# Kernel optimization log

Measured on AMD Instinct MI355X. Metric: run time of the kernel, lower is better.

## Reference

```python
import jax, jax.numpy as jnp
import numpy as np

N_NODES = 5000
N_EDGES = 40000
NUM_ATOM_TYPES = 100
HID = 32            # multiplicity of 0e and 1o in irreps_hidden
EDGE_ATTR_DIM = 8
NUM_BOND_TYPES = 5
OUT_SCALARS = 2 * 6 + 1  # max_charge=6 -> 13x0e
CUTOFF = 5.0
SQRT3 = 1.7320508075688772


def _sh(edge_vec):
    # o3.SphericalHarmonics('1x0e + 1x1o', normalize=True, normalization='component')
    d = jnp.sqrt(jnp.sum(edge_vec * edge_vec, axis=-1) + 1e-12)
    n = edge_vec / d[:, None]
    sh0 = jnp.ones(edge_vec.shape[0], edge_vec.dtype)          # [E]
    sh1 = SQRT3 * n[:, (1, 2, 0)]                              # [E,3], e3nn (y,z,x) order
    return sh0, sh1, d


def _soft_one_hot(d):
    # e3nn.math.soft_one_hot_linspace(d, 0, cutoff, 8, basis='gaussian', cutoff=True)
    values = jnp.linspace(0.0, CUTOFF, EDGE_ATTR_DIM + 2)[1:-1]
    step = CUTOFF / (EDGE_ATTR_DIM + 1)
    diff = (d[:, None] - values[None, :]) / step
    return jnp.exp(-diff * diff) / 1.12


def _mlp(x, W0, b0, W1, b1):
    # ScalarMLP(in, out, hidden=[in], SiLU)
    return jax.nn.silu(x @ W0 + b0) @ W1 + b1


def _tp_init(s, sh0, sh1, w):
    # FCTP(32x0e, 1x0e+1x1o -> 32x0e+32x1o); paths: 0e*0e->0e, 0e*1o->1o
    E = s.shape[0]
    w1 = w[:, : HID * HID].reshape(E, HID, HID)
    w2 = w[:, HID * HID :].reshape(E, HID, HID)
    c = 1.0 / np.sqrt(HID)  # fan-in = 32 per output irrep
    out_s = c * jnp.einsum('eu,euw->ew', s * sh0[:, None], w1)
    out_v = c * jnp.einsum('eu,ei,euw->ewi', s, sh1, w2)
    return out_s, out_v


def _tp_hidden(s, v, sh0, sh1, w):
    # FCTP(32x0e+32x1o, 1x0e+1x1o -> 32x0e+32x1o)
    # path order: 0e*0e->0e, 0e*1o->1o, 1o*0e->1o, 1o*1o->0e
    E = s.shape[0]
    ws = w.reshape(E, 4, HID, HID)
    c = 1.0 / np.sqrt(2 * HID)  # fan-in = 64 per output irrep
    dot = jnp.einsum('eui,ei->eu', v, sh1) / SQRT3  # CG(1,1->0) = delta/sqrt(3)
    out_s = c * (jnp.einsum('eu,euw->ew', s * sh0[:, None], ws[:, 0]) +
                 jnp.einsum('eu,euw->ew', dot, ws[:, 3]))
    out_v = c * (jnp.einsum('eu,ei,euw->ewi', s, sh1, ws[:, 1]) +
                 jnp.einsum('eui,euw->ewi', v * sh0[:, None, None], ws[:, 2]))
    return out_s, out_v


def _edge_tp(s1, v1, s2, v2, sh0, sh1, w):
    # FCTP(64x0e+64x1o (concat of two hidden), 1x0e+1x1o -> 5x0e)
    # blocks in concat order: s_src, v_src, s_dst, v_dst
    E = s1.shape[0]
    ws = w.reshape(E, 4, HID, NUM_BOND_TYPES)
    c = 1.0 / np.sqrt(4 * HID)  # fan-in = 128
    d1 = jnp.einsum('eui,ei->eu', v1, sh1) / SQRT3
    d2 = jnp.einsum('eui,ei->eu', v2, sh1) / SQRT3
    return c * (jnp.einsum('eu,euw->ew', s1 * sh0[:, None], ws[:, 0]) +
                jnp.einsum('eu,euw->ew', d1, ws[:, 1]) +
                jnp.einsum('eu,euw->ew', s2 * sh0[:, None], ws[:, 2]) +
                jnp.einsum('eu,euw->ew', d2, ws[:, 3]))


def _scatter_mean(ms, mv, dst, n):
    cnt = jax.ops.segment_sum(jnp.ones(dst.shape[0], ms.dtype), dst, num_segments=n)
    cnt = jnp.maximum(cnt, 1.0)
    s = jax.ops.segment_sum(ms, dst, num_segments=n) / cnt[:, None]
    v = jax.ops.segment_sum(mv, dst, num_segments=n) / cnt[:, None, None]
    return s, v


def setup_inputs() -> dict:
    key = jax.random.key(0)
    ks = jax.random.split(key, 16)
    def w(k, shape, fan_in):
        return jax.random.normal(k, shape, dtype=jnp.float32) / np.sqrt(fan_in)
    inp = {}
    inp['coordinates'] = jax.random.normal(ks[0], (N_NODES, 3), dtype=jnp.float32) * 1.5
    inp['atom_types'] = jax.random.randint(ks[1], (N_NODES,), 0, NUM_ATOM_TYPES)
    inp['edge_index'] = jax.random.randint(ks[2], (2, N_EDGES), 0, N_NODES)
    inp['atom_embed'] = jax.random.normal(ks[3], (NUM_ATOM_TYPES, HID), dtype=jnp.float32)
    inp['ip_W0'] = w(ks[4], (EDGE_ATTR_DIM, EDGE_ATTR_DIM), EDGE_ATTR_DIM)
    inp['ip_b0'] = jnp.zeros((EDGE_ATTR_DIM,), jnp.float32)
    inp['ip_W1'] = w(ks[5], (EDGE_ATTR_DIM, 2 * HID * HID), EDGE_ATTR_DIM)
    inp['ip_b1'] = jnp.zeros((2 * HID * HID,), jnp.float32)
    inp['ly_W0'] = w(ks[6], (EDGE_ATTR_DIM, EDGE_ATTR_DIM), EDGE_ATTR_DIM)
    inp['ly_b0'] = jnp.zeros((EDGE_ATTR_DIM,), jnp.float32)
    inp['ly_W1'] = w(ks[7], (EDGE_ATTR_DIM, 4 * HID * HID), EDGE_ATTR_DIM)
    inp['ly_b1'] = jnp.zeros((4 * HID * HID,), jnp.float32)
    inp['ly_Ws'] = jax.random.normal(ks[8], (HID, HID), dtype=jnp.float32)
    inp['ly_Wv'] = jax.random.normal(ks[9], (HID, HID), dtype=jnp.float32)
    inp['et_W0'] = w(ks[10], (EDGE_ATTR_DIM, EDGE_ATTR_DIM), EDGE_ATTR_DIM)
    inp['et_b0'] = jnp.zeros((EDGE_ATTR_DIM,), jnp.float32)
    inp['et_W1'] = w(ks[11], (EDGE_ATTR_DIM, 4 * HID * NUM_BOND_TYPES), EDGE_ATTR_DIM)
    inp['et_b1'] = jnp.zeros((4 * HID * NUM_BOND_TYPES,), jnp.float32)
    inp['no_W1'] = jax.random.normal(ks[12], (HID, OUT_SCALARS), dtype=jnp.float32)
    inp['no_W2'] = jax.random.normal(ks[13], (OUT_SCALARS, OUT_SCALARS), dtype=jnp.float32)
    return inp


def reference(coordinates, atom_types, edge_index, atom_embed,
              ip_W0, ip_b0, ip_W1, ip_b1,
              ly_W0, ly_b0, ly_W1, ly_b1, ly_Ws, ly_Wv,
              et_W0, et_b0, et_W1, et_b1, no_W1, no_W2):
    n = coordinates.shape[0]
    src, dst = edge_index[0], edge_index[1]
    edge_vec = coordinates[dst] - coordinates[src]
    sh0, sh1, d = _sh(edge_vec)
    edge_attr = _soft_one_hot(d)                              # [E,8]
    # initial projector: Conv(32x0e -> 32x0e+32x1o)
    s0 = atom_embed[atom_types]                               # [N,32]
    w_ip = _mlp(edge_attr, ip_W0, ip_b0, ip_W1, ip_b1)        # [E,2048]
    ms, mv = _tp_init(s0[src], sh0, sh1, w_ip)
    s, v = _scatter_mean(ms, mv, dst, n)                      # [N,32],[N,32,3]
    # one LinearSelfInteraction(Conv) layer
    w_ly = _mlp(edge_attr, ly_W0, ly_b0, ly_W1, ly_b1)        # [E,4096]
    ms, mv = _tp_hidden(s[src], v[src], sh0, sh1, w_ly)
    cs, cv = _scatter_mean(ms, mv, dst, n)
    lc = 1.0 / np.sqrt(HID)  # e3nn o3.Linear normalization
    s = cs + lc * (s @ ly_Ws)
    v = cv + lc * jnp.einsum('eui,uw->ewi', v, ly_Wv)
    # edge output: FCTP([h_src, h_dst], edge_sh) with radial weights
    w_et = _mlp(edge_attr, et_W0, et_b0, et_W1, et_b1)        # [E,640]
    edge_out = _edge_tp(s[src], v[src], s[dst], v[dst], sh0, sh1, w_et)  # [E,5]
    # node output MLP on detached scalar channel (13x0e)
    sd = jax.lax.stop_gradient(s)
    h = jax.nn.silu(sd @ no_W1 / np.sqrt(HID))
    node_out = h @ no_W2 / np.sqrt(OUT_SCALARS)               # [N,13]
    return edge_out, node_out
```

## Files before the change

### kernel.cpp

```cpp
#include <hip/hip_runtime.h>

#define NN 5000
#define NE 40000

typedef unsigned int u32;
typedef unsigned short u16;
typedef __attribute__((ext_vector_type(8))) short bf16x8;
typedef __attribute__((ext_vector_type(4))) float f32x4;

union ABfrag { uint4 q; bf16x8 v; u32 u[4]; };

__device__ __forceinline__ float siluf(float x) { return x / (1.f + __expf(-x)); }

__device__ __forceinline__ u32 f2bf_u(float f) {
  u32 x = __float_as_uint(f);
  return (x + 0x7FFFu + ((x >> 16) & 1u)) >> 16;
}
__device__ __forceinline__ u16 f2bf(float f) { return (u16)f2bf_u(f); }
__device__ __forceinline__ float bf2f(u16 v) { return __uint_as_float(((u32)v) << 16); }
__device__ __forceinline__ u32 packbf2(float lo, float hi) {
  return f2bf_u(lo) | (f2bf_u(hi) << 16);
}
__device__ __forceinline__ u32 pk2(float a, float b) {
  return ((__float_as_uint(a) + 0x8000u) >> 16) |
         ((__float_as_uint(b) + 0x8000u) & 0xFFFF0000u);
}
__device__ __forceinline__ void pksplit8(const float* p, ABfrag& hi, ABfrag& lo) {
#pragma unroll
  for (int j = 0; j < 8; j += 2) {
    u32 h2 = pk2(p[j], p[j+1]);
    hi.u[j >> 1] = h2;
    float h0 = __uint_as_float(h2 << 16);
    float h1 = __uint_as_float(h2 & 0xFFFF0000u);
    lo.u[j >> 1] = pk2(p[j] - h0, p[j+1] - h1);
  }
}
__device__ __forceinline__ void unpack8(uint4 q, float* f) {
  f[0] = __uint_as_float(q.x << 16); f[1] = __uint_as_float(q.x & 0xFFFF0000u);
  f[2] = __uint_as_float(q.y << 16); f[3] = __uint_as_float(q.y & 0xFFFF0000u);
  f[4] = __uint_as_float(q.z << 16); f[5] = __uint_as_float(q.z & 0xFFFF0000u);
  f[6] = __uint_as_float(q.w << 16); f[7] = __uint_as_float(q.w & 0xFFFF0000u);
}
__device__ __forceinline__ float dot8f(const float* h, const float* w, float init) {
  float a = init;
#pragma unroll
  for (int k = 0; k < 8; k++) a = fmaf(h[k], w[k], a);
  return a;
}
__device__ __forceinline__ void mlp8(const float* ea, const float* __restrict__ W0,
                                     const float* __restrict__ b0, float* h) {
#pragma unroll
  for (int j = 0; j < 8; j++) {
    float a = b0[j];
#pragma unroll
    for (int i = 0; i < 8; i++) a += ea[i] * W0[i*8 + j];
    h[j] = siluf(a);
  }
}

__global__ void k_geom(const float* __restrict__ coords, const int* __restrict__ eidx,
                       const float* __restrict__ ipW0, const float* __restrict__ ipb0,
                       const float* __restrict__ lyW0, const float* __restrict__ lyb0,
                       const float* __restrict__ etW0, const float* __restrict__ etb0,
                       float* __restrict__ sh, float* __restrict__ h_ip,
                       float* __restrict__ h_ly, float* __restrict__ h_et,
                       int* __restrict__ cur, int* __restrict__ perm) {
  int e = blockIdx.x * blockDim.x + threadIdx.x;
  if (e >= NE) return;
  int s = eidx[e], d = eidx[NE + e];
  float vx = coords[d*3+0] - coords[s*3+0];
  float vy = coords[d*3+1] - coords[s*3+1];
  float vz = coords[d*3+2] - coords[s*3+2];
  float dist = sqrtf(vx*vx + vy*vy + vz*vz + 1e-12f);
  float inv = 1.f / dist;
  const float SQ3 = 1.7320508075688772f;
  sh[e*3+0] = SQ3 * vy * inv;
  sh[e*3+1] = SQ3 * vz * inv;
  sh[e*3+2] = SQ3 * vx * inv;
  float ea[8];
  const float step = 5.f / 9.f;
#pragma unroll
  for (int j = 0; j < 8; j++) {
    float diff = (dist - step * (float)(j+1)) * (9.f / 5.f);
    ea[j] = __expf(-diff*diff) * (1.f / 1.12f);
  }
  float h[8];
  mlp8(ea, ipW0, ipb0, h);
#pragma unroll
  for (int j = 0; j < 8; j++) h_ip[e*8+j] = h[j];
  mlp8(ea, lyW0, lyb0, h);
#pragma unroll
  for (int j = 0; j < 8; j++) h_ly[e*8+j] = h[j];
  mlp8(ea, etW0, etb0, h);
#pragma unroll
  for (int j = 0; j < 8; j++) h_et[e*8+j] = h[j];
  int t = atomicAdd(&cur[d], 1);
  if (t < 64) perm[d*64 + t] = e;
}

__global__ __launch_bounds__(256) void k_mconv1(
    const float* __restrict__ hE, const float* __restrict__ sh,
    const float* __restrict__ sIn, const int* __restrict__ atype,
    const int* __restrict__ eidx,
    const float* __restrict__ W1, const float* __restrict__ b1,
    int ldw, float cscale, u16* __restrict__ msg) {
  __shared__ u16 B[64*296];
  {
    int col = threadIdx.x & 63, p = col >> 5, w = col & 31;
    int k0 = (threadIdx.x >> 6) * 72;
    for (int k = k0; k < k0 + 72; k++) {
      float v = (k < 256) ? W1[(k >> 5)*ldw + p*1024 + (k & 31)*32 + w]
                          : b1[p*1024 + (k - 256)*32 + w];
      B[col*296 + k] = f2bf(v);
    }
  }
  __syncthreads();
  int tile = blockIdx.x*4 + (threadIdx.x >> 6);
  if (tile*16 >= NE) return;
  int lane = threadIdx.x & 63;
  int m = lane & 15, q = lane >> 4;
  int e = tile*16 + m;
  int srcn = eidx[e];
  int srow = atype ? atype[srcn] : srcn;
  float4 sA = *(const float4*)&sIn[srow*32 + q*8];
  float4 sB = *(const float4*)&sIn[srow*32 + q*8 + 4];
  float4 hA = *(const float4*)&hE[e*8];
  float4 hB = *(const float4*)&hE[e*8 + 4];
  float sf[8] = {sA.x,sA.y,sA.z,sA.w,sB.x,sB.y,sB.z,sB.w};
  float hf[8] = {hA.x,hA.y,hA.z,hA.w,hB.x,hB.y,hB.z,hB.w};
  f32x4 acc0 = {0.f,0.f,0.f,0.f}, acc1 = acc0, acc2 = acc0, acc3 = acc0;
#pragma unroll
  for (int ks = 0; ks < 9; ks++) {
    float hs = (ks < 8) ? hf[ks] : 1.f;
    float pr[8];
#pragma unroll
    for (int j = 0; j < 8; j++) pr[j] = hs * sf[j];
    ABfrag ahi, alo;
    pksplit8(pr, ahi, alo);
    int kb = ks*32 + q*8;
    ABfrag b0, b1f, b2, b3;
    b0.q  = *(const uint4*)&B[( 0 + m)*296 + kb];
    b1f.q = *(const uint4*)&B[(16 + m)*296 + kb];
    b2.q  = *(const uint4*)&B[(32 + m)*296 + kb];
    b3.q  = *(const uint4*)&B[(48 + m)*296 + kb];
    acc0 = __builtin_amdgcn_mfma_f32_16x16x32_bf16(ahi.v, b0.v,  acc0, 0, 0, 0);
    acc0 = __builtin_amdgcn_mfma_f32_16x16x32_bf16(alo.v, b0.v,  acc0, 0, 0, 0);
    acc1 = __builtin_amdgcn_mfma_f32_16x16x32_bf16(ahi.v, b1f.v, acc1, 0, 0, 0);
    acc1 = __builtin_amdgcn_mfma_f32_16x16x32_bf16(alo.v, b1f.v, acc1, 0, 0, 0);
    acc2 = __builtin_amdgcn_mfma_f32_16x16x32_bf16(ahi.v, b2.v,  acc2, 0, 0, 0);
    acc2 = __builtin_amdgcn_mfma_f32_16x16x32_bf16(alo.v, b2.v,  acc2, 0, 0, 0);
    acc3 = __builtin_amdgcn_mfma_f32_16x16x32_bf16(ahi.v, b3.v,  acc3, 0, 0, 0);
    acc3 = __builtin_amdgcn_mfma_f32_16x16x32_bf16(alo.v, b3.v,  acc3, 0, 0, 0);
  }
#pragma unroll
  for (int r = 0; r < 4; r++) {
    int et = tile*16 + q*4 + r;
    u16* mp = msg + (size_t)et*128;
    mp[m]      = f2bf(cscale*acc0[r]);
    mp[16 + m] = f2bf(cscale*acc1[r]);
    float s0v = sh[et*3+0], s1v = sh[et*3+1], s2v = sh[et*3+2];
    float m0 = cscale*acc2[r], m1 = cscale*acc3[r];
    mp[32 +      m] = f2bf(m0*s0v);
    mp[64 +      m] = f2bf(m0*s1v);
    mp[96 +      m] = f2bf(m0*s2v);
    mp[32 + 16 + m] = f2bf(m1*s0v);
    mp[64 + 16 + m] = f2bf(m1*s1v);
    mp[96 + 16 + m] = f2bf(m1*s2v);
  }
}

__global__ __launch_bounds__(256) void k_conv2(
    const float* __restrict__ hE, const float* __restrict__ sh,
    const float* __restrict__ s1, const float* __restrict__ v1soa,
    const int* __restrict__ eidx,
    const float* __restrict__ W1, const float* __restrict__ b1,
    u16* __restrict__ msgA, u16* __restrict__ msgB) {
  __shared__ u16 B[64*296];
  const bool scalarHalf = blockIdx.x < 625;
  int blk = scalarHalf ? blockIdx.x : blockIdx.x - 625;
  if (scalarHalf) {
    int col = threadIdx.x & 63, p = col >> 5, w = col & 31;
    int k0 = (threadIdx.x >> 6) * 72;
    for (int k = k0; k < k0 + 72; k++) {
      float v = (k < 256) ? W1[(k >> 5)*4096 + p*1024 + (k & 31)*32 + w]
                          : b1[p*1024 + (k - 256)*32 + w];
      B[col*296 + k] = f2bf(v);
    }
  } else {
    int col = threadIdx.x & 63;
    int base = (col < 32) ? (2048 + col) : (3072 + (col - 32));
    int k0 = (threadIdx.x >> 6) * 72;
    for (int k = k0; k < k0 + 72; k++) {
      float v = (k < 256) ? W1[(k >> 5)*4096 + base + (k & 31)*32]
                          : b1[base + (k - 256)*32];
      B[col*296 + k] = f2bf(v);
    }
  }
  __syncthreads();
  int tile = blk*4 + (threadIdx.x >> 6);
  if (tile*16 >= NE) return;
  int lane = threadIdx.x & 63;
  int m = lane & 15, q = lane >> 4;
  int e = tile*16 + m;
  int srcn = eidx[e];
  float4 hA = *(const float4*)&hE[e*8];
  float4 hB = *(const float4*)&hE[e*8 + 4];
  float hf[8] = {hA.x,hA.y,hA.z,hA.w,hB.x,hB.y,hB.z,hB.w};
  const float c = 0.125f;

  if (scalarHalf) {
    float4 sA = *(const float4*)&s1[srcn*32 + q*8];
    float4 sB = *(const float4*)&s1[srcn*32 + q*8 + 4];
    float sf[8] = {sA.x,sA.y,sA.z,sA.w,sB.x,sB.y,sB.z,sB.w};
    f32x4 acc0 = {0.f,0.f,0.f,0.f}, acc1 = acc0, acc2 = acc0, acc3 = acc0;
#pragma unroll
    for (int ks = 0; ks < 9; ks++) {
      float hs = (ks < 8) ? hf[ks] : 1.f;
      float pr[8];
#pragma unroll
      for (int j = 0; j < 8; j++) pr[j] = hs * sf[j];
      ABfrag ahi, alo;
      pksplit8(pr, ahi, alo);
      int kb = ks*32 + q*8;
      ABfrag b0, b1f, b2, b3;
      b0.q  = *(const uint4*)&B[( 0 + m)*296 + kb];
      b1f.q = *(const uint4*)&B[(16 + m)*296 + kb];
      b2.q  = *(const uint4*)&B[(32 + m)*296 + kb];
      b3.q  = *(const uint4*)&B[(48 + m)*296 + kb];
      acc0 = __builtin_amdgcn_mfma_f32_16x16x32_bf16(ahi.v, b0.v,  acc0, 0, 0, 0);
      acc0 = __builtin_amdgcn_mfma_f32_16x16x32_bf16(alo.v, b0.v,  acc0, 0, 0, 0);
      acc1 = __builtin_amdgcn_mfma_f32_16x16x32_bf16(ahi.v, b1f.v, acc1, 0, 0, 0);
      acc1 = __builtin_amdgcn_mfma_f32_16x16x32_bf16(alo.v, b1f.v, acc1, 0, 0, 0);
      acc2 = __builtin_amdgcn_mfma_f32_16x16x32_bf16(ahi.v, b2.v,  acc2, 0, 0, 0);
      acc2 = __builtin_amdgcn_mfma_f32_16x16x32_bf16(alo.v, b2.v,  acc2, 0, 0, 0);
      acc3 = __builtin_amdgcn_mfma_f32_16x16x32_bf16(ahi.v, b3.v,  acc3, 0, 0, 0);
      acc3 = __builtin_amdgcn_mfma_f32_16x16x32_bf16(alo.v, b3.v,  acc3, 0, 0, 0);
    }
#pragma unroll
    for (int r = 0; r < 4; r++) {
      int et = tile*16 + q*4 + r;
      u16* mp = msgA + (size_t)et*128;
      mp[m]      = f2bf(c*acc0[r]);
      mp[16 + m] = f2bf(c*acc1[r]);
      float s0v = sh[et*3+0], s1v = sh[et*3+1], s2v = sh[et*3+2];
      float m0 = c*acc2[r], m1 = c*acc3[r];
      mp[32 +      m] = f2bf(m0*s0v);
      mp[64 +      m] = f2bf(m0*s1v);
      mp[96 +      m] = f2bf(m0*s2v);
      mp[32 + 16 + m] = f2bf(m1*s0v);
      mp[64 + 16 + m] = f2bf(m1*s1v);
      mp[96 + 16 + m] = f2bf(m1*s2v);
    }
  } else {
    const float is3 = 0.5773502691896258f;
    float vf[3][8];
#pragma unroll
    for (int i = 0; i < 3; i++) {
      float4 aa = *(const float4*)&v1soa[i*160000 + srcn*32 + q*8];
      float4 bb = *(const float4*)&v1soa[i*160000 + srcn*32 + q*8 + 4];
      vf[i][0]=aa.x; vf[i][1]=aa.y; vf[i][2]=aa.z; vf[i][3]=aa.w;
      vf[i][4]=bb.x; vf[i][5]=bb.y; vf[i][6]=bb.z; vf[i][7]=bb.w;
    }
    float es0 = sh[e*3+0], es1 = sh[e*3+1], es2 = sh[e*3+2];
    float df[8];
#pragma unroll
    for (int j = 0; j < 8; j++)
      df[j] = (vf[0][j]*es0 + vf[1][j]*es1 + vf[2][j]*es2) * is3;
    f32x4 z = {0.f,0.f,0.f,0.f};
    f32x4 aV00 = z, aV01 = z, aV10 = z, aV11 = z, aV20 = z, aV21 = z, aD0 = z, aD1 = z;
#pragma unroll
    for (int ks = 0; ks < 9; ks++) {
      int kb = ks*32 + q*8;
      ABfrag b0, b1f, b2, b3;
      b0.q  = *(const uint4*)&B[( 0 + m)*296 + kb];
      b1f.q = *(const uint4*)&B[(16 + m)*296 + kb];
      b2.q  = *(const uint4*)&B[(32 + m)*296 + kb];
      b3.q  = *(const uint4*)&B[(48 + m)*296 + kb];
      float hs = (ks < 8) ? hf[ks] : 1.f;
      float pr[8];
      ABfrag hi, lo;
#pragma unroll
      for (int j = 0; j < 8; j++) pr[j] = hs * vf[0][j];
      pksplit8(pr, hi, lo);
      aV00 = __builtin_amdgcn_mfma_f32_16x16x32_bf16(hi.v, b0.v,  aV00, 0, 0, 0);
      aV00 = __builtin_amdgcn_mfma_f32_16x16x32_bf16(lo.v, b0.v,  aV00, 0, 0, 0);
      aV01 = __builtin_amdgcn_mfma_f32_16x16x32_bf16(hi.v, b1f.v, aV01, 0, 0, 0);
      aV01 = __builtin_amdgcn_mfma_f32_16x16x32_bf16(lo.v, b1f.v, aV01, 0, 0, 0);
#pragma unroll
      for (int j = 0; j < 8; j++) pr[j] = hs * vf[1][j];
      pksplit8(pr, hi, lo);
      aV10 = __builtin_amdgcn_mfma_f32_16x16x32_bf16(hi.v, b0.v,  aV10, 0, 0, 0);
      aV10 = __builtin_amdgcn_mfma_f32_16x16x32_bf16(lo.v, b0.v,  aV10, 0, 0, 0);
      aV11 = __builtin_amdgcn_mfma_f32_16x16x32_bf16(hi.v, b1f.v, aV11, 0, 0, 0);
      aV11 = __builtin_amdgcn_mfma_f32_16x16x32_bf16(lo.v, b1f.v, aV11, 0, 0, 0);
#pragma unroll
      for (int j = 0; j < 8; j++) pr[j] = hs * vf[2][j];
      pksplit8(pr, hi, lo);
      aV20 = __builtin_amdgcn_mfma_f32_16x16x32_bf16(hi.v, b0.v,  aV20, 0, 0, 0);
      aV20 = __builtin_amdgcn_mfma_f32_16x16x32_bf16(lo.v, b0.v,  aV20, 0, 0, 0);
      aV21 = __builtin_amdgcn_mfma_f32_16x16x32_bf16(hi.v, b1f.v, aV21, 0, 0, 0);
      aV21 = __builtin_amdgcn_mfma_f32_16x16x32_bf16(lo.v, b1f.v, aV21, 0, 0, 0);
#pragma unroll
      for (int j = 0; j < 8; j++) pr[j] = hs * df[j];
      pksplit8(pr, hi, lo);
      aD0  = __builtin_amdgcn_mfma_f32_16x16x32_bf16(hi.v, b2.v,  aD0,  0, 0, 0);
      aD0  = __builtin_amdgcn_mfma_f32_16x16x32_bf16(lo.v, b2.v,  aD0,  0, 0, 0);
      aD1  = __builtin_amdgcn_mfma_f32_16x16x32_bf16(hi.v, b3.v,  aD1,  0, 0, 0);
      aD1  = __builtin_amdgcn_mfma_f32_16x16x32_bf16(lo.v, b3.v,  aD1,  0, 0, 0);
    }
#pragma unroll
    for (int r = 0; r < 4; r++) {
      int et = tile*16 + q*4 + r;
      u16* mp = msgB + (size_t)et*128;
      mp[m]      = f2bf(c*aD0[r]);
      mp[16 + m] = f2bf(c*aD1[r]);
      mp[32 +      m] = f2bf(c*aV00[r]);
      mp[32 + 16 + m] = f2bf(c*aV01[r]);
      mp[64 +      m] = f2bf(c*aV10[r]);
      mp[64 + 16 + m] = f2bf(c*aV11[r]);
      mp[96 +      m] = f2bf(c*aV20[r]);
      mp[96 + 16 + m] = f2bf(c*aV21[r]);
    }
  }
}

__global__ void k_gather1(const u16* __restrict__ msg, const int* __restrict__ perm,
                          const int* __restrict__ cur, float* __restrict__ s1,
                          float* __restrict__ v1soa) {
  int t = blockIdx.x * blockDim.x + threadIdx.x;
  int n = t >> 7, c = t & 127;
  if (n >= NN) return;
  int deg = min(cur[n], 64);
  float acc = 0.f;
  for (int j = 0; j < deg; j++) {
    int e = perm[n*64 + j];
    acc += bf2f(msg[(size_t)e*128 + c]);
  }
  acc /= (float)max(deg, 1);
  if (c < 32) s1[n*32 + c] = acc;
  else { int i = (c-32) >> 5, w = (c-32) & 31; v1soa[i*160000 + n*32 + w] = acc; }
}

__global__ __launch_bounds__(256) void k_gather2(
    const u16* __restrict__ msgA, const u16* __restrict__ msgB,
    const int* __restrict__ perm, const int* __restrict__ cur,
    const float* __restrict__ s1, const float* __restrict__ v1soa,
    const float* __restrict__ Ws, const float* __restrict__ Wv,
    const float* __restrict__ noW1, const float* __restrict__ noW2,
    float* __restrict__ s2, float* __restrict__ v2, float* __restrict__ outN) {
  __shared__ float sb[2][32];
  __shared__ float hb[2][13];
  int t = blockIdx.x * blockDim.x + threadIdx.x;
  int n = t >> 7, c = t & 127;
  int ln = (threadIdx.x >> 7);
  int deg = min(cur[n], 64);
  float acc = 0.f;
  for (int j = 0; j < deg; j++) {
    int e = perm[n*64 + j];
    acc += bf2f(msgA[(size_t)e*128 + c]) + bf2f(msgB[(size_t)e*128 + c]);
  }
  acc /= (float)max(deg, 1);
  const float lc = 0.17677669529663687f;
  if (c < 32) {
    float ss = 0.f;
#pragma unroll 8
    for (int u = 0; u < 32; u++) ss += s1[n*32 + u] * Ws[u*32 + c];
    float val = acc + lc*ss;
    s2[n*32 + c] = val;
    sb[ln][c] = val;
  } else {
    int i = (c-32) >> 5, w = (c-32) & 31;
    float sv = 0.f;
#pragma unroll 8
    for (int u = 0; u < 32; u++) sv += v1soa[i*160000 + n*32 + u] * Wv[u*32 + w];
    v2[n*96 + w*3 + i] = acc + lc*sv;
  }
  __syncthreads();
  const float i32 = 0.17677669529663687f;
  if (c < 13) {
    float a = 0.f;
#pragma unroll 8
    for (int u = 0; u < 32; u++) a += sb[ln][u] * noW1[u*13 + c];
    hb[ln][c] = siluf(a * i32);
  }
  __syncthreads();
  const float i13 = 0.2773500981126146f;
  if (c < 13) {
    float a = 0.f;
#pragma unroll
    for (int j = 0; j < 13; j++) a += hb[ln][j] * noW2[j*13 + c];
    outN[n*13 + c] = a * i13;
  }
}

__global__ __launch_bounds__(256) void k_e3(
    const float* __restrict__ hE, const float* __restrict__ sh,
    const float* __restrict__ s2, const float* __restrict__ v2,
    const int* __restrict__ eidx,
    const float* __restrict__ W1, const float* __restrict__ b1,
    float* __restrict__ out) {
  __shared__ uint4 WQ[640];
  __shared__ float BQ[640];
  for (int t = threadIdx.x; t < 640; t += 256) {
    int u = t & 31, pw = t >> 5, p2 = pw / 5, w = pw - p2*5;
    int col = p2*160 + u*5 + w;
    const float* s = W1 + col;
    uint4 q;
    q.x = packbf2(s[0],      s[640]);
    q.y = packbf2(s[1280],   s[1920]);
    q.z = packbf2(s[2560],   s[3200]);
    q.w = packbf2(s[3840],   s[4480]);
    WQ[t] = q;
    BQ[t] = b1[col];
  }
  __syncthreads();
  const int g = threadIdx.x >> 5, tw = threadIdx.x & 31;
  const float c = 0.08838834764831845f;
  const float is3 = 0.5773502691896258f;
  for (int p = blockIdx.x*8 + g; p*2 < NE; p += gridDim.x*8) {
    int e0 = p*2, e1 = e0 + 1;
    float h0[8], h1[8];
    {
      float4 qa = *(const float4*)&hE[e0*8];
      float4 qb = *(const float4*)&hE[e0*8+4];
      h0[0]=qa.x; h0[1]=qa.y; h0[2]=qa.z; h0[3]=qa.w;
      h0[4]=qb.x; h0[5]=qb.y; h0[6]=qb.z; h0[7]=qb.w;
      float4 qc = *(const float4*)&hE[e1*8];
      float4 qd = *(const float4*)&hE[e1*8+4];
      h1[0]=qc.x; h1[1]=qc.y; h1[2]=qc.z; h1[3]=qc.w;
      h1[4]=qd.x; h1[5]=qd.y; h1[6]=qd.z; h1[7]=qd.w;
    }
    int sA = eidx[e0], dA = eidx[NE+e0];
    int sB = eidx[e1], dB = eidx[NE+e1];
    float sa0 = sh[e0*3+0], sa1 = sh[e0*3+1], sa2 = sh[e0*3+2];
    float sb0 = sh[e1*3+0], sb1 = sh[e1*3+1], sb2 = sh[e1*3+2];
    float c00 = s2[sA*32 + tw];
    float c01 = (v2[sA*96+tw*3+0]*sa0 + v2[sA*96+tw*3+1]*sa1 + v2[sA*96+tw*3+2]*sa2) * is3;
    float c02 = s2[dA*32 + tw];
    float c03 = (v2[dA*96+tw*3+0]*sa0 + v2[dA*96+tw*3+1]*sa1 + v2[dA*96+tw*3+2]*sa2) * is3;
    float c10 = s2[sB*32 + tw];
    float c11 = (v2[sB*96+tw*3+0]*sb0 + v2[sB*96+tw*3+1]*sb1 + v2[sB*96+tw*3+2]*sb2) * is3;
    float c12 = s2[dB*32 + tw];
    float c13 = (v2[dB*96+tw*3+0]*sb0 + v2[dB*96+tw*3+1]*sb1 + v2[dB*96+tw*3+2]*sb2) * is3;
    float part0[5] = {0,0,0,0,0};
    float part1[5] = {0,0,0,0,0};
#pragma unroll
    for (int pp = 0; pp < 4; pp++) {
      float cp0 = (pp==0) ? c00 : (pp==1) ? c01 : (pp==2) ? c02 : c03;
      float cp1 = (pp==0) ? c10 : (pp==1) ? c11 : (pp==2) ? c12 : c13;
#pragma unroll
      for (int w = 0; w < 5; w++) {
        int idx = (pp*5 + w)*32 + tw;
        float f[8];
        unpack8(WQ[idx], f);
        float bv = BQ[idx];
        part0[w] = fmaf(cp0, dot8f(h0, f, bv), part0[w]);
        part1[w] = fmaf(cp1, dot8f(h1, f, bv), part1[w]);
      }
    }
#pragma unroll
    for (int off = 16; off > 0; off >>= 1)
#pragma unroll
      for (int w = 0; w < 5; w++) {
        part0[w] += __shfl_xor(part0[w], off, 32);
        part1[w] += __shfl_xor(part1[w], off, 32);
      }
    float outv = 0.f;
#pragma unroll
    for (int w = 0; w < 5; w++) {
      if (tw == w)     outv = part0[w];
      if (tw == 5 + w) outv = part1[w];
    }
    if (tw < 10) out[e0*5 + tw] = c * outv;
  }
}

extern "C" void kernel_launch(void* const* d_in, const int* in_sizes, int n_in,
                              void* d_out, int out_size, void* d_ws, size_t ws_size,
                              hipStream_t stream) {
  (void)in_sizes; (void)n_in; (void)out_size; (void)ws_size;
  const float* coords = (const float*)d_in[0];
  const int*   atype  = (const int*)d_in[1];
  const int*   eidx   = (const int*)d_in[2];
  const float* emb    = (const float*)d_in[3];
  const float* ipW0 = (const float*)d_in[4];
  const float* ipb0 = (const float*)d_in[5];
  const float* ipW1 = (const float*)d_in[6];
  const float* ipb1 = (const float*)d_in[7];
  const float* lyW0 = (const float*)d_in[8];
  const float* lyb0 = (const float*)d_in[9];
  const float* lyW1 = (const float*)d_in[10];
  const float* lyb1 = (const float*)d_in[11];
  const float* lyWs = (const float*)d_in[12];
  const float* lyWv = (const float*)d_in[13];
  const float* etW0 = (const float*)d_in[14];
  const float* etb0 = (const float*)d_in[15];
  const float* etW1 = (const float*)d_in[16];
  const float* etb1 = (const float*)d_in[17];
  const float* noW1 = (const float*)d_in[18];
  const float* noW2 = (const float*)d_in[19];

  float* ws = (float*)d_ws;
  float* sh    = ws;
  float* h_ip  = ws + 120000;
  float* h_ly  = ws + 440000;
  float* h_et  = ws + 760000;
  float* s1    = ws + 1240000;
  float* v1soa = ws + 1400000;
  float* s2    = ws + 1880000;
  float* v2    = ws + 2040000;
  int*   cur   = (int*)(ws + 2520000);
  int*   perm  = (int*)(ws + 2525000);
  u16*   msgA  = (u16*)(ws + 2845000);
  u16*   msgB  = (u16*)(ws + 5405000);

  float* outE = (float*)d_out;
  float* outN = (float*)d_out + NE*5;

  hipMemsetAsync(cur, 0, (size_t)NN * sizeof(int), stream);
  k_geom<<<(NE + 255)/256, 256, 0, stream>>>(coords, eidx, ipW0, ipb0, lyW0, lyb0,
                                             etW0, etb0, sh, h_ip, h_ly, h_et, cur, perm);
  k_mconv1<<<625, 256, 0, stream>>>(h_ip, sh, emb, atype, eidx, ipW1, ipb1, 2048,
                                    0.17677669529663687f, msgA);
  k_gather1<<<(NN*128 + 255)/256, 256, 0, stream>>>(msgA, perm, cur, s1, v1soa);
  k_conv2<<<1250, 256, 0, stream>>>(h_ly, sh, s1, v1soa, eidx, lyW1, lyb1, msgA, msgB);
  k_gather2<<<2500, 256, 0, stream>>>(msgA, msgB, perm, cur, s1, v1soa,
                                      lyWs, lyWv, noW1, noW2, s2, v2, outN);
  k_e3<<<1024, 256, 0, stream>>>(h_et, sh, s2, v2, eidx, etW1, etb1, outE);
}
```

Baseline: 205.1 us.

## Switch conv MFMA to single-pass fp16 with persistent blocks and fragment-major LDS

```diff
diff --git a/kernel.cpp b/kernel.cpp
--- a/kernel.cpp
+++ b/kernel.cpp
@@ -5,10 +5,11 @@
 
 typedef unsigned int u32;
 typedef unsigned short u16;
-typedef __attribute__((ext_vector_type(8))) short bf16x8;
+typedef __fp16 h16x2 __attribute__((ext_vector_type(2)));
+typedef _Float16 f16x8 __attribute__((ext_vector_type(8)));
 typedef __attribute__((ext_vector_type(4))) float f32x4;
 
-union ABfrag { uint4 q; bf16x8 v; u32 u[4]; };
+union AF { u32 u[4]; f16x8 v; uint4 q; };
 
 __device__ __forceinline__ float siluf(float x) { return x / (1.f + __expf(-x)); }
 
@@ -21,19 +22,14 @@
 __device__ __forceinline__ u32 packbf2(float lo, float hi) {
   return f2bf_u(lo) | (f2bf_u(hi) << 16);
 }
-__device__ __forceinline__ u32 pk2(float a, float b) {
-  return ((__float_as_uint(a) + 0x8000u) >> 16) |
-         ((__float_as_uint(b) + 0x8000u) & 0xFFFF0000u);
-}
-__device__ __forceinline__ void pksplit8(const float* p, ABfrag& hi, ABfrag& lo) {
-#pragma unroll
-  for (int j = 0; j < 8; j += 2) {
-    u32 h2 = pk2(p[j], p[j+1]);
-    hi.u[j >> 1] = h2;
-    float h0 = __uint_as_float(h2 << 16);
-    float h1 = __uint_as_float(h2 & 0xFFFF0000u);
-    lo.u[j >> 1] = pk2(p[j] - h0, p[j+1] - h1);
-  }
+__device__ __forceinline__ u32 pkh2(float a, float b) {
+  union { h16x2 h; u32 u; } r;
+  r.h = __builtin_amdgcn_cvt_pkrtz(a, b);
+  return r.u;
+}
+__device__ __forceinline__ u16 f2h(float v) {
+  _Float16 h = (_Float16)v;
+  return *(u16*)&h;
 }
 __device__ __forceinline__ void unpack8(uint4 q, float* f) {
   f[0] = __uint_as_float(q.x << 16); f[1] = __uint_as_float(q.x & 0xFFFF0000u);
@@ -56,6 +52,14 @@
     for (int i = 0; i < 8; i++) a += ea[i] * W0[i*8 + j];
     h[j] = siluf(a);
   }
+}
+__device__ __forceinline__ AF mkfrag(float hs, const float* s) {
+  AF a;
+  a.u[0] = pkh2(hs*s[0], hs*s[1]);
+  a.u[1] = pkh2(hs*s[2], hs*s[3]);
+  a.u[2] = pkh2(hs*s[4], hs*s[5]);
+  a.u[3] = pkh2(hs*s[6], hs*s[7]);
+  return a;
 }
 
 __global__ void k_geom(const float* __restrict__ coords, const int* __restrict__ eidx,
@@ -104,222 +108,182 @@
     const int* __restrict__ eidx,
     const float* __restrict__ W1, const float* __restrict__ b1,
     int ldw, float cscale, u16* __restrict__ msg) {
-  __shared__ u16 B[64*296];
+  __shared__ __align__(16) u16 B2[36*64*8];
   {
     int col = threadIdx.x & 63, p = col >> 5, w = col & 31;
     int k0 = (threadIdx.x >> 6) * 72;
     for (int k = k0; k < k0 + 72; k++) {
       float v = (k < 256) ? W1[(k >> 5)*ldw + p*1024 + (k & 31)*32 + w]
                           : b1[p*1024 + (k - 256)*32 + w];
-      B[col*296 + k] = f2bf(v);
+      B2[((k >> 3)*64 + col)*8 + (k & 7)] = f2h(v);
     }
   }
   __syncthreads();
-  int tile = blockIdx.x*4 + (threadIdx.x >> 6);
-  if (tile*16 >= NE) return;
   int lane = threadIdx.x & 63;
-  int m = lane & 15, q = lane >> 4;
-  int e = tile*16 + m;
-  int srcn = eidx[e];
-  int srow = atype ? atype[srcn] : srcn;
-  float4 sA = *(const float4*)&sIn[srow*32 + q*8];
-  float4 sB = *(const float4*)&sIn[srow*32 + q*8 + 4];
-  float4 hA = *(const float4*)&hE[e*8];
-  float4 hB = *(const float4*)&hE[e*8 + 4];
-  float sf[8] = {sA.x,sA.y,sA.z,sA.w,sB.x,sB.y,sB.z,sB.w};
-  float hf[8] = {hA.x,hA.y,hA.z,hA.w,hB.x,hB.y,hB.z,hB.w};
-  f32x4 acc0 = {0.f,0.f,0.f,0.f}, acc1 = acc0, acc2 = acc0, acc3 = acc0;
-#pragma unroll
-  for (int ks = 0; ks < 9; ks++) {
-    float hs = (ks < 8) ? hf[ks] : 1.f;
-    float pr[8];
-#pragma unroll
-    for (int j = 0; j < 8; j++) pr[j] = hs * sf[j];
-    ABfrag ahi, alo;
-    pksplit8(pr, ahi, alo);
-    int kb = ks*32 + q*8;
-    ABfrag b0, b1f, b2, b3;
-    b0.q  = *(const uint4*)&B[( 0 + m)*296 + kb];
-    b1f.q = *(const uint4*)&B[(16 + m)*296 + kb];
-    b2.q  = *(const uint4*)&B[(32 + m)*296 + kb];
-    b3.q  = *(const uint4*)&B[(48 + m)*296 + kb];
-    acc0 = __builtin_amdgcn_mfma_f32_16x16x32_bf16(ahi.v, b0.v,  acc0, 0, 0, 0);
-    acc0 = __builtin_amdgcn_mfma_f32_16x16x32_bf16(alo.v, b0.v,  acc0, 0, 0, 0);
-    acc1 = __builtin_amdgcn_mfma_f32_16x16x32_bf16(ahi.v, b1f.v, acc1, 0, 0, 0);
-    acc1 = __builtin_amdgcn_mfma_f32_16x16x32_bf16(alo.v, b1f.v, acc1, 0, 0, 0);
-    acc2 = __builtin_amdgcn_mfma_f32_16x16x32_bf16(ahi.v, b2.v,  acc2, 0, 0, 0);
-    acc2 = __builtin_amdgcn_mfma_f32_16x16x32_bf16(alo.v, b2.v,  acc2, 0, 0, 0);
-    acc3 = __builtin_amdgcn_mfma_f32_16x16x32_bf16(ahi.v, b3.v,  acc3, 0, 0, 0);
-    acc3 = __builtin_amdgcn_mfma_f32_16x16x32_bf16(alo.v, b3.v,  acc3, 0, 0, 0);
-  }
-#pragma unroll
-  for (int r = 0; r < 4; r++) {
-    int et = tile*16 + q*4 + r;
-    u16* mp = msg + (size_t)et*128;
-    mp[m]      = f2bf(cscale*acc0[r]);
-    mp[16 + m] = f2bf(cscale*acc1[r]);
-    float s0v = sh[et*3+0], s1v = sh[et*3+1], s2v = sh[et*3+2];
-    float m0 = cscale*acc2[r], m1 = cscale*acc3[r];
-    mp[32 +      m] = f2bf(m0*s0v);
-    mp[64 +      m] = f2bf(m0*s1v);
-    mp[96 +      m] = f2bf(m0*s2v);
-    mp[32 + 16 + m] = f2bf(m1*s0v);
-    mp[64 + 16 + m] = f2bf(m1*s1v);
-    mp[96 + 16 + m] = f2bf(m1*s2v);
-  }
-}
-
+  int m = lane & 15, q = lane >> 4, wid = threadIdx.x >> 6;
+  for (int tile = blockIdx.x*4 + wid; tile*16 < NE; tile += gridDim.x*4) {
+    int e = tile*16 + m;
+    int srcn = eidx[e];
+    int srow = atype ? atype[srcn] : srcn;
+    float4 sA = *(const float4*)&sIn[srow*32 + q*8];
+    float4 sB = *(const float4*)&sIn[srow*32 + q*8 + 4];
+    float4 hA = *(const float4*)&hE[e*8];
+    float4 hB = *(const float4*)&hE[e*8 + 4];
+    float sf[8] = {sA.x,sA.y,sA.z,sA.w,sB.x,sB.y,sB.z,sB.w};
+    float hf[8] = {hA.x,hA.y,hA.z,hA.w,hB.x,hB.y,hB.z,hB.w};
+    f32x4 acc0 = {0.f,0.f,0.f,0.f}, acc1 = acc0, acc2 = acc0, acc3 = acc0;
+#pragma unroll
+    for (int ks = 0; ks < 9; ks++) {
+      float hs = (ks < 8) ? hf[ks] : 1.f;
+      AF a = mkfrag(hs, sf);
+      int c2 = (ks*4 + q)*64;
+      AF b0, b1f, b2, b3;
+      b0.q  = *(const uint4*)&B2[(c2 +  0 + m)*8];
+      b1f.q = *(const uint4*)&B2[(c2 + 16 + m)*8];
+      b2.q  = *(const uint4*)&B2[(c2 + 32 + m)*8];
+      b3.q  = *(const uint4*)&B2[(c2 + 48 + m)*8];
+      acc0 = __builtin_amdgcn_mfma_f32_16x16x32_f16(a.v, b0.v,  acc0, 0, 0, 0);
+      acc1 = __builtin_amdgcn_mfma_f32_16x16x32_f16(a.v, b1f.v, acc1, 0, 0, 0);
+      acc2 = __builtin_amdgcn_mfma_f32_16x16x32_f16(a.v, b2.v,  acc2, 0, 0, 0);
+      acc3 = __builtin_amdgcn_mfma_f32_16x16x32_f16(a.v, b3.v,  acc3, 0, 0, 0);
+    }
+#pragma unroll
+    for (int r = 0; r < 4; r++) {
+      int et = tile*16 + q*4 + r;
+      u16* mp = msg + (size_t)et*128;
+      mp[m]      = f2bf(cscale*acc0[r]);
+      mp[16 + m] = f2bf(cscale*acc1[r]);
+      float s0v = sh[et*3+0], s1v = sh[et*3+1], s2v = sh[et*3+2];
+      float m0 = cscale*acc2[r], m1 = cscale*acc3[r];
+      mp[32 +      m] = f2bf(m0*s0v);
+      mp[64 +      m] = f2bf(m0*s1v);
+      mp[96 +      m] = f2bf(m0*s2v);
+      mp[32 + 16 + m] = f2bf(m1*s0v);
+      mp[64 + 16 + m] = f2bf(m1*s1v);
+      mp[96 + 16 + m] = f2bf(m1*s2v);
+    }
+  }
+}
+
+#define HB 320
 __global__ __launch_bounds__(256) void k_conv2(
     const float* __restrict__ hE, const float* __restrict__ sh,
     const float* __restrict__ s1, const float* __restrict__ v1soa,
     const int* __restrict__ eidx,
     const float* __restrict__ W1, const float* __restrict__ b1,
     u16* __restrict__ msgA, u16* __restrict__ msgB) {
-  __shared__ u16 B[64*296];
-  const bool scalarHalf = blockIdx.x < 625;
-  int blk = scalarHalf ? blockIdx.x : blockIdx.x - 625;
-  if (scalarHalf) {
-    int col = threadIdx.x & 63, p = col >> 5, w = col & 31;
-    int k0 = (threadIdx.x >> 6) * 72;
-    for (int k = k0; k < k0 + 72; k++) {
-      float v = (k < 256) ? W1[(k >> 5)*4096 + p*1024 + (k & 31)*32 + w]
-                          : b1[p*1024 + (k - 256)*32 + w];
-      B[col*296 + k] = f2bf(v);
-    }
-  } else {
+  __shared__ __align__(16) u16 B2[36*64*8];
+  const bool scalarHalf = blockIdx.x < HB;
+  int blk = scalarHalf ? blockIdx.x : blockIdx.x - HB;
+  {
     int col = threadIdx.x & 63;
-    int base = (col < 32) ? (2048 + col) : (3072 + (col - 32));
+    int base = scalarHalf ? ((col >> 5)*1024 + (col & 31))
+                          : ((col < 32) ? (2048 + col) : (3072 + (col - 32)));
     int k0 = (threadIdx.x >> 6) * 72;
     for (int k = k0; k < k0 + 72; k++) {
       float v = (k < 256) ? W1[(k >> 5)*4096 + base + (k & 31)*32]
                           : b1[base + (k - 256)*32];
-      B[col*296 + k] = f2bf(v);
+      B2[((k >> 3)*64 + col)*8 + (k & 7)] = f2h(v);
     }
   }
   __syncthreads();
-  int tile = blk*4 + (threadIdx.x >> 6);
-  if (tile*16 >= NE) return;
   int lane = threadIdx.x & 63;
-  int m = lane & 15, q = lane >> 4;
-  int e = tile*16 + m;
-  int srcn = eidx[e];
-  float4 hA = *(const float4*)&hE[e*8];
-  float4 hB = *(const float4*)&hE[e*8 + 4];
-  float hf[8] = {hA.x,hA.y,hA.z,hA.w,hB.x,hB.y,hB.z,hB.w};
+  int m = lane & 15, q = lane >> 4, wid = threadIdx.x >> 6;
   const float c = 0.125f;
-
-  if (scalarHalf) {
-    float4 sA = *(const float4*)&s1[srcn*32 + q*8];
-    float4 sB = *(const float4*)&s1[srcn*32 + q*8 + 4];
-    float sf[8] = {sA.x,sA.y,sA.z,sA.w,sB.x,sB.y,sB.z,sB.w};
-    f32x4 acc0 = {0.f,0.f,0.f,0.f}, acc1 = acc0, acc2 = acc0, acc3 = acc0;
-#pragma unroll
-    for (int ks = 0; ks < 9; ks++) {
-      float hs = (ks < 8) ? hf[ks] : 1.f;
-      float pr[8];
-#pragma unroll
-      for (int j = 0; j < 8; j++) pr[j] = hs * sf[j];
-      ABfrag ahi, alo;
-      pksplit8(pr, ahi, alo);
-      int kb = ks*32 + q*8;
-      ABfrag b0, b1f, b2, b3;
-      b0.q  = *(const uint4*)&B[( 0 + m)*296 + kb];
-      b1f.q = *(const uint4*)&B[(16 + m)*296 + kb];
-      b2.q  = *(const uint4*)&B[(32 + m)*296 + kb];
-      b3.q  = *(const uint4*)&B[(48 + m)*296 + kb];
-      acc0 = __builtin_amdgcn_mfma_f32_16x16x32_bf16(ahi.v, b0.v,  acc0, 0, 0, 0);
-      acc0 = __builtin_amdgcn_mfma_f32_16x16x32_bf16(alo.v, b0.v,  acc0, 0, 0, 0);
-      acc1 = __builtin_amdgcn_mfma_f32_16x16x32_bf16(ahi.v, b1f.v, acc1, 0, 0, 0);
-      acc1 = __builtin_amdgcn_mfma_f32_16x16x32_bf16(alo.v, b1f.v, acc1, 0, 0, 0);
-      acc2 = __builtin_amdgcn_mfma_f32_16x16x32_bf16(ahi.v, b2.v,  acc2, 0, 0, 0);
-      acc2 = __builtin_amdgcn_mfma_f32_16x16x32_bf16(alo.v, b2.v,  acc2, 0, 0, 0);
-      acc3 = __builtin_amdgcn_mfma_f32_16x16x32_bf16(ahi.v, b3.v,  acc3, 0, 0, 0);
-      acc3 = __builtin_amdgcn_mfma_f32_16x16x32_bf16(alo.v, b3.v,  acc3, 0, 0, 0);
-    }
-#pragma unroll
-    for (int r = 0; r < 4; r++) {
-      int et = tile*16 + q*4 + r;
-      u16* mp = msgA + (size_t)et*128;
-      mp[m]      = f2bf(c*acc0[r]);
-      mp[16 + m] = f2bf(c*acc1[r]);
-      float s0v = sh[et*3+0], s1v = sh[et*3+1], s2v = sh[et*3+2];
-      float m0 = c*acc2[r], m1 = c*acc3[r];
-      mp[32 +      m] = f2bf(m0*s0v);
-      mp[64 +      m] = f2bf(m0*s1v);
-      mp[96 +      m] = f2bf(m0*s2v);
-      mp[32 + 16 + m] = f2bf(m1*s0v);
-      mp[64 + 16 + m] = f2bf(m1*s1v);
-      mp[96 + 16 + m] = f2bf(m1*s2v);
-    }
-  } else {
-    const float is3 = 0.5773502691896258f;
-    float vf[3][8];
-#pragma unroll
-    for (int i = 0; i < 3; i++) {
-      float4 aa = *(const float4*)&v1soa[i*160000 + srcn*32 + q*8];
-      float4 bb = *(const float4*)&v1soa[i*160000 + srcn*32 + q*8 + 4];
-      vf[i][0]=aa.x; vf[i][1]=aa.y; vf[i][2]=aa.z; vf[i][3]=aa.w;
-      vf[i][4]=bb.x; vf[i][5]=bb.y; vf[i][6]=bb.z; vf[i][7]=bb.w;
-    }
-    float es0 = sh[e*3+0], es1 = sh[e*3+1], es2 = sh[e*3+2];
-    float df[8];
-#pragma unroll
-    for (int j = 0; j < 8; j++)
-      df[j] = (vf[0][j]*es0 + vf[1][j]*es1 + vf[2][j]*es2) * is3;
-    f32x4 z = {0.f,0.f,0.f,0.f};
-    f32x4 aV00 = z, aV01 = z, aV10 = z, aV11 = z, aV20 = z, aV21 = z, aD0 = z, aD1 = z;
-#pragma unroll
-    for (int ks = 0; ks < 9; ks++) {
-      int kb = ks*32 + q*8;
-      ABfrag b0, b1f, b2, b3;
-      b0.q  = *(const uint4*)&B[( 0 + m)*296 + kb];
-      b1f.q = *(const uint4*)&B[(16 + m)*296 + kb];
-      b2.q  = *(const uint4*)&B[(32 + m)*296 + kb];
-      b3.q  = *(const uint4*)&B[(48 + m)*296 + kb];
-      float hs = (ks < 8) ? hf[ks] : 1.f;
-      float pr[8];
-      ABfrag hi, lo;
-#pragma unroll
-      for (int j = 0; j < 8; j++) pr[j] = hs * vf[0][j];
-      pksplit8(pr, hi, lo);
-      aV00 = __builtin_amdgcn_mfma_f32_16x16x32_bf16(hi.v, b0.v,  aV00, 0, 0, 0);
-      aV00 = __builtin_amdgcn_mfma_f32_16x16x32_bf16(lo.v, b0.v,  aV00, 0, 0, 0);
-      aV01 = __builtin_amdgcn_mfma_f32_16x16x32_bf16(hi.v, b1f.v, aV01, 0, 0, 0);
-      aV01 = __builtin_amdgcn_mfma_f32_16x16x32_bf16(lo.v, b1f.v, aV01, 0, 0, 0);
-#pragma unroll
-      for (int j = 0; j < 8; j++) pr[j] = hs * vf[1][j];
-      pksplit8(pr, hi, lo);
-      aV10 = __builtin_amdgcn_mfma_f32_16x16x32_bf16(hi.v, b0.v,  aV10, 0, 0, 0);
-      aV10 = __builtin_amdgcn_mfma_f32_16x16x32_bf16(lo.v, b0.v,  aV10, 0, 0, 0);
-      aV11 = __builtin_amdgcn_mfma_f32_16x16x32_bf16(hi.v, b1f.v, aV11, 0, 0, 0);
-      aV11 = __builtin_amdgcn_mfma_f32_16x16x32_bf16(lo.v, b1f.v, aV11, 0, 0, 0);
-#pragma unroll
-      for (int j = 0; j < 8; j++) pr[j] = hs * vf[2][j];
-      pksplit8(pr, hi, lo);
-      aV20 = __builtin_amdgcn_mfma_f32_16x16x32_bf16(hi.v, b0.v,  aV20, 0, 0, 0);
-      aV20 = __builtin_amdgcn_mfma_f32_16x16x32_bf16(lo.v, b0.v,  aV20, 0, 0, 0);
-      aV21 = __builtin_amdgcn_mfma_f32_16x16x32_bf16(hi.v, b1f.v, aV21, 0, 0, 0);
-      aV21 = __builtin_amdgcn_mfma_f32_16x16x32_bf16(lo.v, b1f.v, aV21, 0, 0, 0);
-#pragma unroll
-      for (int j = 0; j < 8; j++) pr[j] = hs * df[j];
-      pksplit8(pr, hi, lo);
-      aD0  = __builtin_amdgcn_mfma_f32_16x16x32_bf16(hi.v, b2.v,  aD0,  0, 0, 0);
-      aD0  = __builtin_amdgcn_mfma_f32_16x16x32_bf16(lo.v, b2.v,  aD0,  0, 0, 0);
-      aD1  = __builtin_amdgcn_mfma_f32_16x16x32_bf16(hi.v, b3.v,  aD1,  0, 0, 0);
-      aD1  = __builtin_amdgcn_mfma_f32_16x16x32_bf16(lo.v, b3.v,  aD1,  0, 0, 0);
-    }
-#pragma unroll
-    for (int r = 0; r < 4; r++) {
-      int et = tile*16 + q*4 + r;
-      u16* mp = msgB + (size_t)et*128;
-      mp[m]      = f2bf(c*aD0[r]);
-      mp[16 + m] = f2bf(c*aD1[r]);
-      mp[32 +      m] = f2bf(c*aV00[r]);
-      mp[32 + 16 + m] = f2bf(c*aV01[r]);
-      mp[64 +      m] = f2bf(c*aV10[r]);
-      mp[64 + 16 + m] = f2bf(c*aV11[r]);
-      mp[96 +      m] = f2bf(c*aV20[r]);
-      mp[96 + 16 + m] = f2bf(c*aV21[r]);
+  for (int tile = blk*4 + wid; tile*16 < NE; tile += HB*4) {
+    int e = tile*16 + m;
+    int srcn = eidx[e];
+    float4 hA = *(const float4*)&hE[e*8];
+    float4 hB = *(const float4*)&hE[e*8 + 4];
+    float hf[8] = {hA.x,hA.y,hA.z,hA.w,hB.x,hB.y,hB.z,hB.w};
+
+    if (scalarHalf) {
+      float4 sA = *(const float4*)&s1[srcn*32 + q*8];
+      float4 sB = *(const float4*)&s1[srcn*32 + q*8 + 4];
+      float sf[8] = {sA.x,sA.y,sA.z,sA.w,sB.x,sB.y,sB.z,sB.w};
+      f32x4 acc0 = {0.f,0.f,0.f,0.f}, acc1 = acc0, acc2 = acc0, acc3 = acc0;
+#pragma unroll
+      for (int ks = 0; ks < 9; ks++) {
+        float hs = (ks < 8) ? hf[ks] : 1.f;
+        AF a = mkfrag(hs, sf);
+        int c2 = (ks*4 + q)*64;
+        AF b0, b1f, b2, b3;
+        b0.q  = *(const uint4*)&B2[(c2 +  0 + m)*8];
+        b1f.q = *(const uint4*)&B2[(c2 + 16 + m)*8];
+        b2.q  = *(const uint4*)&B2[(c2 + 32 + m)*8];
+        b3.q  = *(const uint4*)&B2[(c2 + 48 + m)*8];
+        acc0 = __builtin_amdgcn_mfma_f32_16x16x32_f16(a.v, b0.v,  acc0, 0, 0, 0);
+        acc1 = __builtin_amdgcn_mfma_f32_16x16x32_f16(a.v, b1f.v, acc1, 0, 0, 0);
+        acc2 = __builtin_amdgcn_mfma_f32_16x16x32_f16(a.v, b2.v,  acc2, 0, 0, 0);
+        acc3 = __builtin_amdgcn_mfma_f32_16x16x32_f16(a.v, b3.v,  acc3, 0, 0, 0);
+      }
+#pragma unroll
+      for (int r = 0; r < 4; r++) {
+        int et = tile*16 + q*4 + r;
+        u16* mp = msgA + (size_t)et*128;
+        mp[m]      = f2bf(c*acc0[r]);
+        mp[16 + m] = f2bf(c*acc1[r]);
+        float s0v = sh[et*3+0], s1v = sh[et*3+1], s2v = sh[et*3+2];
+        float m0 = c*acc2[r], m1 = c*acc3[r];
+        mp[32 +      m] = f2bf(m0*s0v);
+        mp[64 +      m] = f2bf(m0*s1v);
+        mp[96 +      m] = f2bf(m0*s2v);
+        mp[32 + 16 + m] = f2bf(m1*s0v);
+        mp[64 + 16 + m] = f2bf(m1*s1v);
+        mp[96 + 16 + m] = f2bf(m1*s2v);
+      }
+    } else {
+      const float is3 = 0.5773502691896258f;
+      float vf[3][8];
+#pragma unroll
+      for (int i = 0; i < 3; i++) {
+        float4 aa = *(const float4*)&v1soa[i*160000 + srcn*32 + q*8];
+        float4 bb = *(const float4*)&v1soa[i*160000 + srcn*32 + q*8 + 4];
+        vf[i][0]=aa.x; vf[i][1]=aa.y; vf[i][2]=aa.z; vf[i][3]=aa.w;
+        vf[i][4]=bb.x; vf[i][5]=bb.y; vf[i][6]=bb.z; vf[i][7]=bb.w;
+      }
+      float es0 = sh[e*3+0], es1 = sh[e*3+1], es2 = sh[e*3+2];
+      float df[8];
+#pragma unroll
+      for (int j = 0; j < 8; j++)
+        df[j] = (vf[0][j]*es0 + vf[1][j]*es1 + vf[2][j]*es2) * is3;
+      f32x4 z = {0.f,0.f,0.f,0.f};
+      f32x4 aV00 = z, aV01 = z, aV10 = z, aV11 = z, aV20 = z, aV21 = z, aD0 = z, aD1 = z;
+#pragma unroll
+      for (int ks = 0; ks < 9; ks++) {
+        float hs = (ks < 8) ? hf[ks] : 1.f;
+        int c2 = (ks*4 + q)*64;
+        AF b0, b1f, b2, b3;
+        b0.q  = *(const uint4*)&B2[(c2 +  0 + m)*8];
+        b1f.q = *(const uint4*)&B2[(c2 + 16 + m)*8];
+        b2.q  = *(const uint4*)&B2[(c2 + 32 + m)*8];
+        b3.q  = *(const uint4*)&B2[(c2 + 48 + m)*8];
+        AF a0 = mkfrag(hs, vf[0]);
+        AF a1 = mkfrag(hs, vf[1]);
+        AF a2 = mkfrag(hs, vf[2]);
+        AF ad = mkfrag(hs, df);
+        aV00 = __builtin_amdgcn_mfma_f32_16x16x32_f16(a0.v, b0.v,  aV00, 0, 0, 0);
+        aV01 = __builtin_amdgcn_mfma_f32_16x16x32_f16(a0.v, b1f.v, aV01, 0, 0, 0);
+        aV10 = __builtin_amdgcn_mfma_f32_16x16x32_f16(a1.v, b0.v,  aV10, 0, 0, 0);
+        aV11 = __builtin_amdgcn_mfma_f32_16x16x32_f16(a1.v, b1f.v, aV11, 0, 0, 0);
+        aV20 = __builtin_amdgcn_mfma_f32_16x16x32_f16(a2.v, b0.v,  aV20, 0, 0, 0);
+        aV21 = __builtin_amdgcn_mfma_f32_16x16x32_f16(a2.v, b1f.v, aV21, 0, 0, 0);
+        aD0  = __builtin_amdgcn_mfma_f32_16x16x32_f16(ad.v, b2.v,  aD0,  0, 0, 0);
+        aD1  = __builtin_amdgcn_mfma_f32_16x16x32_f16(ad.v, b3.v,  aD1,  0, 0, 0);
+      }
+#pragma unroll
+      for (int r = 0; r < 4; r++) {
+        int et = tile*16 + q*4 + r;
+        u16* mp = msgB + (size_t)et*128;
+        mp[m]      = f2bf(c*aD0[r]);
+        mp[16 + m] = f2bf(c*aD1[r]);
+        mp[32 +      m] = f2bf(c*aV00[r]);
+        mp[32 + 16 + m] = f2bf(c*aV01[r]);
+        mp[64 +      m] = f2bf(c*aV10[r]);
+        mp[64 + 16 + m] = f2bf(c*aV11[r]);
+        mp[96 +      m] = f2bf(c*aV20[r]);
+        mp[96 + 16 + m] = f2bf(c*aV21[r]);
+      }
     }
   }
 }
@@ -517,13 +481,13 @@
   float* outE = (float*)d_out;
   float* outN = (float*)d_out + NE*5;
 
-  hipMemsetAsync(cur, 0, (size_t)NN * sizeof(int), stream);
+  (void)hipMemsetAsync(cur, 0, (size_t)NN * sizeof(int), stream);
   k_geom<<<(NE + 255)/256, 256, 0, stream>>>(coords, eidx, ipW0, ipb0, lyW0, lyb0,
                                              etW0, etb0, sh, h_ip, h_ly, h_et, cur, perm);
-  k_mconv1<<<625, 256, 0, stream>>>(h_ip, sh, emb, atype, eidx, ipW1, ipb1, 2048,
-                                    0.17677669529663687f, msgA);
+  k_mconv1<<<HB, 256, 0, stream>>>(h_ip, sh, emb, atype, eidx, ipW1, ipb1, 2048,
+                                   0.17677669529663687f, msgA);
   k_gather1<<<(NN*128 + 255)/256, 256, 0, stream>>>(msgA, perm, cur, s1, v1soa);
-  k_conv2<<<1250, 256, 0, stream>>>(h_ly, sh, s1, v1soa, eidx, lyW1, lyb1, msgA, msgB);
+  k_conv2<<<2*HB, 256, 0, stream>>>(h_ly, sh, s1, v1soa, eidx, lyW1, lyb1, msgA, msgB);
   k_gather2<<<2500, 256, 0, stream>>>(msgA, msgB, perm, cur, s1, v1soa,
                                       lyWs, lyWv, noW1, noW2, s2, v2, outN);
   k_e3<<<1024, 256, 0, stream>>>(h_et, sh, s2, v2, eidx, etW1, etb1, outE);
```

After: 191.7 us. 6.6% less time.
